# Optimization experiments

Hardware: AMD Instinct MI355X
Metric: run time of the kernel (lower is better)

The kernel has to match this reference:

```python
import jax, jax.numpy as jnp
import numpy as np

H = 64  # hidden_size

def _lstm_layer(x_tbi, h0, c0, w_ih, w_hh, b_ih, b_hh):
    """x_tbi: [T,B,I]; returns (out [T,B,H], h_n [B,H], c_n [B,H]).
    PyTorch gate order: i, f, g, o."""
    b = b_ih + b_hh  # [4H]
    # Precompute input projections for all timesteps at once (memory-friendly GEMM)
    xg = jnp.einsum('tbi,gi->tbg', x_tbi, w_ih) + b  # [T,B,4H]

    def step(carry, xg_t):
        h, c = carry
        gates = xg_t + h @ w_hh.T  # [B,4H]
        i, f, g, o = jnp.split(gates, 4, axis=-1)
        i = jax.nn.sigmoid(i)
        f = jax.nn.sigmoid(f)
        g = jnp.tanh(g)
        o = jax.nn.sigmoid(o)
        c = f * c + i * g
        h = o * jnp.tanh(c)
        return (h, c), h

    (h_n, c_n), out = jax.lax.scan(step, (h0, c0), xg)
    return out, h_n, c_n


def setup_inputs() -> dict:
    key = jax.random.key(0)
    B, T, I, O = 256, 1024, 128, 128
    ks = jax.random.split(key, 12)
    s_ih0 = 1.0 / np.sqrt(H)
    inp = {
        'x': jax.random.normal(ks[0], (B, T, I), dtype=jnp.float32),
        'h0': jnp.zeros((2, B, H), dtype=jnp.float32),
        'c0': jnp.zeros((2, B, H), dtype=jnp.float32),
        'w_ih0': jax.random.uniform(ks[1], (4 * H, I), jnp.float32, -s_ih0, s_ih0),
        'w_hh0': jax.random.uniform(ks[2], (4 * H, H), jnp.float32, -s_ih0, s_ih0),
        'b_ih0': jax.random.uniform(ks[3], (4 * H,), jnp.float32, -s_ih0, s_ih0),
        'b_hh0': jax.random.uniform(ks[4], (4 * H,), jnp.float32, -s_ih0, s_ih0),
        'w_ih1': jax.random.uniform(ks[5], (4 * H, H), jnp.float32, -s_ih0, s_ih0),
        'w_hh1': jax.random.uniform(ks[6], (4 * H, H), jnp.float32, -s_ih0, s_ih0),
        'b_ih1': jax.random.uniform(ks[7], (4 * H,), jnp.float32, -s_ih0, s_ih0),
        'b_hh1': jax.random.uniform(ks[8], (4 * H,), jnp.float32, -s_ih0, s_ih0),
        'w_fc': jax.random.uniform(ks[9], (O, H), jnp.float32, -s_ih0, s_ih0),
        'b_fc': jax.random.uniform(ks[10], (O,), jnp.float32, -s_ih0, s_ih0),
    }
    return inp


def reference(x, h0, c0, w_ih0, w_hh0, b_ih0, b_hh0, w_ih1, w_hh1, b_ih1, b_hh1, w_fc, b_fc):
    # x: [B,T,I] (batch_first) -> time-major [T,B,I]
    x_tbi = jnp.swapaxes(x, 0, 1)
    out0, h0n, c0n = _lstm_layer(x_tbi, h0[0], c0[0], w_ih0, w_hh0, b_ih0, b_hh0)
    # Dropout(p=0.5) between layers is identity in eval mode.
    out1, h1n, c1n = _lstm_layer(out0, h0[1], c0[1], w_ih1, w_hh1, b_ih1, b_hh1)
    out = jnp.swapaxes(out1, 0, 1)  # [B,T,H]
    flat = out.reshape(-1, H)  # [B*T, H]
    logits = flat @ w_fc.T + b_fc  # [B*T, O]
    h_n = jnp.stack([h0n, h1n], axis=0)  # [2,B,H]
    c_n = jnp.stack([c0n, c1n], axis=0)
    return logits, (h_n, c_n)
```

## Files before the change

kernel.cpp:

```cpp
#include <hip/hip_runtime.h>

#define T_STEPS 1024
#define BATCH   256
#define HSZ     64
#define OSZ     128

__device__ __forceinline__ float fast_rcp(float x) { return __builtin_amdgcn_rcpf(x); }
__device__ __forceinline__ float tanhf_(float x) {
    float e = __expf(2.0f * x);
    return fmaf(-2.0f, fast_rcp(e + 1.0f), 1.0f);
}


extern "C" __global__ void __launch_bounds__(512, 2)
lstm_l0(const float* __restrict__ x,
        const float* __restrict__ h0,
        const float* __restrict__ c0,
        const float* __restrict__ w_ih,
        const float* __restrict__ w_hh,
        const float* __restrict__ b_ih,
        const float* __restrict__ b_hh,
        float* __restrict__ out0,
        float* __restrict__ hn, float* __restrict__ cn)
{
    const int t_ = threadIdx.x;
    const int b  = blockIdx.x;
    const int j  = t_ >> 3;
    const int gt = (t_ >> 1) & 3;
    const int hf = t_ & 1;
    const int row = gt * HSZ + j;

    __shared__ __align__(16) float xbuf[64 * 128];
    __shared__ __align__(16) float obuf[64 * HSZ];
    __shared__ __align__(16) float hbuf[2][HSZ];

    float wih[64], whh[32];
    {
        const float4* wr = reinterpret_cast<const float4*>(w_ih + (size_t)row * 128 + hf * 64);
        #pragma unroll
        for (int k = 0; k < 16; ++k) { float4 v = wr[k];
            wih[4*k+0]=v.x; wih[4*k+1]=v.y; wih[4*k+2]=v.z; wih[4*k+3]=v.w; }
        const float4* wr2 = reinterpret_cast<const float4*>(w_hh + (size_t)row * 64 + hf * 32);
        #pragma unroll
        for (int k = 0; k < 8; ++k) { float4 v = wr2[k];
            whh[4*k+0]=v.x; whh[4*k+1]=v.y; whh[4*k+2]=v.z; whh[4*k+3]=v.w; }
    }
    const float bias = b_ih[row] + b_hh[row];
    const float am = (gt == 2) ? -2.0f : -1.0f;
    const float aa = (gt == 2) ?  2.0f :  1.0f;
    const float ab = (gt == 2) ? -1.0f :  0.0f;

    float c = c0[(size_t)b * HSZ + j];
    float h = 0.0f;
    if ((t_ & 7) == 0) hbuf[0][j] = h0[(size_t)b * HSZ + j];

    for (int t = 0; t < T_STEPS; ++t) {
        const int tc = t & 63;
        const int p  = t & 1;
        if (tc == 0) {
            if (t) {
                float4* dst = reinterpret_cast<float4*>(out0 + ((size_t)b * T_STEPS + (t - 64)) * HSZ);
                const float4* s4 = reinterpret_cast<const float4*>(obuf);
                #pragma unroll
                for (int k = 0; k < 2; ++k) dst[t_ + 512 * k] = s4[t_ + 512 * k];
            }
            const float4* src = reinterpret_cast<const float4*>(x + ((size_t)b * T_STEPS + t) * 128);
            float4* dxt = reinterpret_cast<float4*>(xbuf);
            #pragma unroll
            for (int k = 0; k < 4; ++k) dxt[t_ + 512 * k] = src[t_ + 512 * k];
            __syncthreads();
        }

        const float4* xv = reinterpret_cast<const float4*>(xbuf + tc * 128 + hf * 64);
        const float4* hv = reinterpret_cast<const float4*>(&hbuf[p][hf * 32]);
        float a0 = 0.f, a1 = 0.f, a2 = 0.f, a3 = 0.f;
        #pragma unroll
        for (int k = 0; k < 16; ++k) { float4 v = xv[k];
            a0 = fmaf(v.x, wih[4*k+0], a0);
            a1 = fmaf(v.y, wih[4*k+1], a1);
            a2 = fmaf(v.z, wih[4*k+2], a2);
            a3 = fmaf(v.w, wih[4*k+3], a3); }
        #pragma unroll
        for (int k = 0; k < 8; ++k) { float4 v = hv[k];
            a0 = fmaf(v.x, whh[4*k+0], a0);
            a1 = fmaf(v.y, whh[4*k+1], a1);
            a2 = fmaf(v.z, whh[4*k+2], a2);
            a3 = fmaf(v.w, whh[4*k+3], a3); }
        float part = (a0 + a1) + (a2 + a3);
        float pre  = part + __shfl_xor(part, 1) + bias;

        float act = fmaf(aa, fast_rcp(1.0f + __expf(am * pre)), ab);

        float q1 = __shfl_xor(act, 2);
        float q2 = __shfl_xor(act, 4);
        float q3 = __shfl_xor(q1, 4);
        const bool b0 = (gt & 1), b1 = (gt & 2);
        float lo  = b0 ? q1  : act;
        float hi  = b0 ? q3  : q2;
        float lo2 = b0 ? act : q1;
        float hi2 = b0 ? q2  : q3;
        float iv = b1 ? hi  : lo;
        float fv = b1 ? hi2 : lo2;
        float gv = b1 ? lo  : hi;
        float ov = b1 ? lo2 : hi2;

        c = fmaf(fv, c, iv * gv);
        h = ov * tanhf_(c);
        if ((t_ & 7) == 0) { hbuf[p ^ 1][j] = h; obuf[tc * HSZ + j] = h; }
        __syncthreads();
    }

    {
        float4* dst = reinterpret_cast<float4*>(out0 + ((size_t)b * T_STEPS + (T_STEPS - 64)) * HSZ);
        const float4* s4 = reinterpret_cast<const float4*>(obuf);
        #pragma unroll
        for (int k = 0; k < 2; ++k) dst[t_ + 512 * k] = s4[t_ + 512 * k];
    }
    if ((t_ & 7) == 0) {
        hn[(size_t)b * HSZ + j] = h;
        cn[(size_t)b * HSZ + j] = c;
    }
}

extern "C" __global__ void __launch_bounds__(512, 2)
lstm_l1_fc(const float* __restrict__ in0,
           const float* __restrict__ h0, const float* __restrict__ c0,
           const float* __restrict__ w_ih,
           const float* __restrict__ w_hh,
           const float* __restrict__ b_ih, const float* __restrict__ b_hh,
           const float* __restrict__ w_fc,
           const float* __restrict__ b_fc,
           float* __restrict__ logits,
           float* __restrict__ hn, float* __restrict__ cn)
{
    const int t_ = threadIdx.x;
    const int b  = blockIdx.x;
    const int j  = t_ >> 3;
    const int gt = (t_ >> 1) & 3;
    const int hf = t_ & 1;
    const int row = gt * HSZ + j;
    const int o  = t_ >> 2;
    const int q  = t_ & 3;

    __shared__ __align__(16) float ibuf[64 * HSZ];
    __shared__ __align__(16) float lbuf[64 * OSZ];
    __shared__ __align__(16) float hbuf[2][HSZ];

    float wih[32], whh[32], wfc[16];
    {
        const float4* wr = reinterpret_cast<const float4*>(w_ih + (size_t)row * 64 + hf * 32);
        #pragma unroll
        for (int k = 0; k < 8; ++k) { float4 v = wr[k];
            wih[4*k+0]=v.x; wih[4*k+1]=v.y; wih[4*k+2]=v.z; wih[4*k+3]=v.w; }
        const float4* wr2 = reinterpret_cast<const float4*>(w_hh + (size_t)row * 64 + hf * 32);
        #pragma unroll
        for (int k = 0; k < 8; ++k) { float4 v = wr2[k];
            whh[4*k+0]=v.x; whh[4*k+1]=v.y; whh[4*k+2]=v.z; whh[4*k+3]=v.w; }
        const float4* wr3 = reinterpret_cast<const float4*>(w_fc + (size_t)o * 64 + q * 16);
        #pragma unroll
        for (int k = 0; k < 4; ++k) { float4 v = wr3[k];
            wfc[4*k+0]=v.x; wfc[4*k+1]=v.y; wfc[4*k+2]=v.z; wfc[4*k+3]=v.w; }
    }
    const float bias = b_ih[row] + b_hh[row];
    const float bfc  = b_fc[o];
    const float am = (gt == 2) ? -2.0f : -1.0f;
    const float aa = (gt == 2) ?  2.0f :  1.0f;
    const float ab = (gt == 2) ? -1.0f :  0.0f;

    float c = c0[(size_t)b * HSZ + j];
    float h = 0.0f;
    if ((t_ & 7) == 0) hbuf[0][j] = h0[(size_t)b * HSZ + j];

    for (int t = 0; t < T_STEPS; ++t) {
        const int tc = t & 63;
        const int p  = t & 1;

        if (t) {
            float f0 = 0.f;
            const float4* hv4 = reinterpret_cast<const float4*>(&hbuf[p][q * 16]);
            #pragma unroll
            for (int k = 0; k < 4; ++k) { float4 v = hv4[k];
                f0 = fmaf(v.x, wfc[4*k+0], f0);
                f0 = fmaf(v.y, wfc[4*k+1], f0);
                f0 = fmaf(v.z, wfc[4*k+2], f0);
                f0 = fmaf(v.w, wfc[4*k+3], f0); }
            f0 += __shfl_xor(f0, 1);
            f0 += __shfl_xor(f0, 2);
            int slot = (tc == 0) ? 63 : (tc - 1);
            if (q == 0) lbuf[slot * OSZ + o] = f0 + bfc;
        }

        if (tc == 0) {
            if (t) {
                __syncthreads();
                float4* dst = reinterpret_cast<float4*>(logits + ((size_t)b * T_STEPS + (t - 64)) * OSZ);
                const float4* s4 = reinterpret_cast<const float4*>(lbuf);
                #pragma unroll
                for (int k = 0; k < 4; ++k) dst[t_ + 512 * k] = s4[t_ + 512 * k];
            }
            const float4* src = reinterpret_cast<const float4*>(in0 + ((size_t)b * T_STEPS + t) * HSZ);
            float4* dxt = reinterpret_cast<float4*>(ibuf);
            #pragma unroll
            for (int k = 0; k < 2; ++k) dxt[t_ + 512 * k] = src[t_ + 512 * k];
            __syncthreads();
        }

        const float4* xv = reinterpret_cast<const float4*>(ibuf + tc * HSZ + hf * 32);
        const float4* hv = reinterpret_cast<const float4*>(&hbuf[p][hf * 32]);
        float a0 = 0.f, a1 = 0.f, a2 = 0.f, a3 = 0.f;
        #pragma unroll
        for (int k = 0; k < 8; ++k) { float4 v = xv[k];
            a0 = fmaf(v.x, wih[4*k+0], a0);
            a1 = fmaf(v.y, wih[4*k+1], a1);
            a2 = fmaf(v.z, wih[4*k+2], a2);
            a3 = fmaf(v.w, wih[4*k+3], a3); }
        #pragma unroll
        for (int k = 0; k < 8; ++k) { float4 v = hv[k];
            a0 = fmaf(v.x, whh[4*k+0], a0);
            a1 = fmaf(v.y, whh[4*k+1], a1);
            a2 = fmaf(v.z, whh[4*k+2], a2);
            a3 = fmaf(v.w, whh[4*k+3], a3); }
        float part = (a0 + a1) + (a2 + a3);
        float pre  = part + __shfl_xor(part, 1) + bias;

        float act = fmaf(aa, fast_rcp(1.0f + __expf(am * pre)), ab);
        float q1 = __shfl_xor(act, 2);
        float q2 = __shfl_xor(act, 4);
        float q3 = __shfl_xor(q1, 4);
        const bool b0 = (gt & 1), b1 = (gt & 2);
        float lo  = b0 ? q1  : act;
        float hi  = b0 ? q3  : q2;
        float lo2 = b0 ? act : q1;
        float hi2 = b0 ? q2  : q3;
        float iv = b1 ? hi  : lo;
        float fv = b1 ? hi2 : lo2;
        float gv = b1 ? lo  : hi;
        float ov = b1 ? lo2 : hi2;

        c = fmaf(fv, c, iv * gv);
        h = ov * tanhf_(c);
        if ((t_ & 7) == 0) hbuf[p ^ 1][j] = h;
        __syncthreads();
    }

    {
        float f0 = 0.f;
        const float4* hv4 = reinterpret_cast<const float4*>(&hbuf[0][q * 16]);
        #pragma unroll
        for (int k = 0; k < 4; ++k) { float4 v = hv4[k];
            f0 = fmaf(v.x, wfc[4*k+0], f0);
            f0 = fmaf(v.y, wfc[4*k+1], f0);
            f0 = fmaf(v.z, wfc[4*k+2], f0);
            f0 = fmaf(v.w, wfc[4*k+3], f0); }
        f0 += __shfl_xor(f0, 1);
        f0 += __shfl_xor(f0, 2);
        if (q == 0) lbuf[63 * OSZ + o] = f0 + bfc;
        __syncthreads();
        float4* dst = reinterpret_cast<float4*>(logits + ((size_t)b * T_STEPS + (T_STEPS - 64)) * OSZ);
        const float4* s4 = reinterpret_cast<const float4*>(lbuf);
        #pragma unroll
        for (int k = 0; k < 4; ++k) dst[t_ + 512 * k] = s4[t_ + 512 * k];
    }
    if ((t_ & 7) == 0) {
        hn[(size_t)b * HSZ + j] = h;
        cn[(size_t)b * HSZ + j] = c;
    }
}

extern "C" void kernel_launch(void* const* d_in, const int* in_sizes, int n_in,
                              void* d_out, int out_size, void* d_ws, size_t ws_size,
                              hipStream_t stream) {
    const float* x     = (const float*)d_in[0];
    const float* h0    = (const float*)d_in[1];
    const float* c0    = (const float*)d_in[2];
    const float* w_ih0 = (const float*)d_in[3];
    const float* w_hh0 = (const float*)d_in[4];
    const float* b_ih0 = (const float*)d_in[5];
    const float* b_hh0 = (const float*)d_in[6];
    const float* w_ih1 = (const float*)d_in[7];
    const float* w_hh1 = (const float*)d_in[8];
    const float* b_ih1 = (const float*)d_in[9];
    const float* b_hh1 = (const float*)d_in[10];
    const float* w_fc  = (const float*)d_in[11];
    const float* b_fc  = (const float*)d_in[12];

    float* out = (float*)d_out;
    const size_t n_logits = (size_t)BATCH * T_STEPS * OSZ;
    const size_t n_state  = (size_t)BATCH * HSZ;
    float* logits = out;
    float* hn     = out + n_logits;
    float* cn     = hn + 2 * n_state;

    float* out0 = (float*)d_ws;

    lstm_l0<<<BATCH, 512, 0, stream>>>(
        x, h0, c0, w_ih0, w_hh0, b_ih0, b_hh0, out0, hn, cn);

    lstm_l1_fc<<<BATCH, 512, 0, stream>>>(
        out0, h0 + n_state, c0 + n_state,
        w_ih1, w_hh1, b_ih1, b_hh1, w_fc, b_fc,
        logits, hn + n_state, cn + n_state);
}
```

Before: 1.817 ms.

## Split block into scan and producer warps to pipeline input projection off critical path

```diff
diff --git a/kernel.cpp b/kernel.cpp
--- a/kernel.cpp
+++ b/kernel.cpp
@@ -1,122 +1,145 @@
 #include <hip/hip_runtime.h>
 
 #define T_STEPS 1024
-#define BATCH   256
 #define HSZ     64
 #define OSZ     128
 
+typedef float4 F4;
+
 __device__ __forceinline__ float fast_rcp(float x) { return __builtin_amdgcn_rcpf(x); }
-__device__ __forceinline__ float tanhf_(float x) {
+__device__ __forceinline__ float tanh_fast(float x) {
     float e = __expf(2.0f * x);
     return fmaf(-2.0f, fast_rcp(e + 1.0f), 1.0f);
 }
 
+#define DOT(W, i) { F4 v_ = vs[i]; \
+    a0 = fmaf(v_.x, (W).x, a0); a1 = fmaf(v_.y, (W).y, a1); \
+    a2 = fmaf(v_.z, (W).z, a2); a3 = fmaf(v_.w, (W).w, a3); }
+
+#define GATE_SELECT(act, gt, iv, fv, gv, ov) \
+    float q1 = __shfl_xor((act), 1); \
+    float q2 = __shfl_xor((act), 2); \
+    float q3 = __shfl_xor(q1, 2); \
+    const bool b0 = (gt) & 1, b1 = (gt) & 2; \
+    float iv = b1 ? (b0 ? q3 : q2) : (b0 ? q1 : (act)); \
+    float fv = b1 ? (b0 ? q2 : q3) : (b0 ? (act) : q1); \
+    float gv = b1 ? (b0 ? q1 : (act)) : (b0 ? q3 : q2); \
+    float ov = b1 ? (b0 ? (act) : q1) : (b0 ? q2 : q3);
 
 extern "C" __global__ void __launch_bounds__(512, 2)
 lstm_l0(const float* __restrict__ x,
-        const float* __restrict__ h0,
-        const float* __restrict__ c0,
+        const float* __restrict__ h0, const float* __restrict__ c0,
         const float* __restrict__ w_ih,
         const float* __restrict__ w_hh,
-        const float* __restrict__ b_ih,
-        const float* __restrict__ b_hh,
+        const float* __restrict__ b_ih, const float* __restrict__ b_hh,
         float* __restrict__ out0,
         float* __restrict__ hn, float* __restrict__ cn)
 {
     const int t_ = threadIdx.x;
     const int b  = blockIdx.x;
-    const int j  = t_ >> 3;
-    const int gt = (t_ >> 1) & 3;
-    const int hf = t_ & 1;
-    const int row = gt * HSZ + j;
+    const bool isScan = (t_ < 256);
+    const int u  = t_ & 255;
+    const int j  = u >> 2;
+    const int gt = u & 3;
 
     __shared__ __align__(16) float xbuf[64 * 128];
-    __shared__ __align__(16) float obuf[64 * HSZ];
+    __shared__ __align__(16) float obuf[2][64 * HSZ];
+    __shared__ __align__(16) float xg[2][256];
     __shared__ __align__(16) float hbuf[2][HSZ];
 
-    float wih[64], whh[32];
-    {
-        const float4* wr = reinterpret_cast<const float4*>(w_ih + (size_t)row * 128 + hf * 64);
-        #pragma unroll
-        for (int k = 0; k < 16; ++k) { float4 v = wr[k];
-            wih[4*k+0]=v.x; wih[4*k+1]=v.y; wih[4*k+2]=v.z; wih[4*k+3]=v.w; }
-        const float4* wr2 = reinterpret_cast<const float4*>(w_hh + (size_t)row * 64 + hf * 32);
-        #pragma unroll
-        for (int k = 0; k < 8; ++k) { float4 v = wr2[k];
-            whh[4*k+0]=v.x; whh[4*k+1]=v.y; whh[4*k+2]=v.z; whh[4*k+3]=v.w; }
-    }
-    const float bias = b_ih[row] + b_hh[row];
+    F4 W00,W01,W02,W03,W04,W05,W06,W07,W08,W09,W10,W11,W12,W13,W14,W15;
+    F4 W16,W17,W18,W19,W20,W21,W22,W23,W24,W25,W26,W27,W28,W29,W30,W31;
+    {
+        const F4 z = {0.f, 0.f, 0.f, 0.f};
+        if (isScan) {
+            const F4* ws = reinterpret_cast<const F4*>(w_hh + (size_t)(gt * HSZ + j) * HSZ);
+            W00=ws[0]; W01=ws[1]; W02=ws[2];  W03=ws[3];  W04=ws[4];  W05=ws[5];  W06=ws[6];  W07=ws[7];
+            W08=ws[8]; W09=ws[9]; W10=ws[10]; W11=ws[11]; W12=ws[12]; W13=ws[13]; W14=ws[14]; W15=ws[15];
+            W16=z; W17=z; W18=z; W19=z; W20=z; W21=z; W22=z; W23=z;
+            W24=z; W25=z; W26=z; W27=z; W28=z; W29=z; W30=z; W31=z;
+        } else {
+            const F4* ws = reinterpret_cast<const F4*>(w_ih + (size_t)u * 128);
+            W00=ws[0];  W01=ws[1];  W02=ws[2];  W03=ws[3];  W04=ws[4];  W05=ws[5];  W06=ws[6];  W07=ws[7];
+            W08=ws[8];  W09=ws[9];  W10=ws[10]; W11=ws[11]; W12=ws[12]; W13=ws[13]; W14=ws[14]; W15=ws[15];
+            W16=ws[16]; W17=ws[17]; W18=ws[18]; W19=ws[19]; W20=ws[20]; W21=ws[21]; W22=ws[22]; W23=ws[23];
+            W24=ws[24]; W25=ws[25]; W26=ws[26]; W27=ws[27]; W28=ws[28]; W29=ws[29]; W30=ws[30]; W31=ws[31];
+        }
+    }
+    const float bias = isScan ? 0.f : (b_ih[u] + b_hh[u]);
     const float am = (gt == 2) ? -2.0f : -1.0f;
     const float aa = (gt == 2) ?  2.0f :  1.0f;
     const float ab = (gt == 2) ? -1.0f :  0.0f;
 
-    float c = c0[(size_t)b * HSZ + j];
-    float h = 0.0f;
-    if ((t_ & 7) == 0) hbuf[0][j] = h0[(size_t)b * HSZ + j];
+    float c = 0.f, h = 0.f;
+    if (isScan) {
+        c = c0[(size_t)b * HSZ + j];
+        if (gt == 0) hbuf[0][j] = h0[(size_t)b * HSZ + j];
+    }
+    {
+        const F4* src = reinterpret_cast<const F4*>(x + (size_t)b * T_STEPS * 128);
+        F4* dst = reinterpret_cast<F4*>(xbuf);
+        #pragma unroll
+        for (int k = 0; k < 4; ++k) dst[t_ + 512 * k] = src[t_ + 512 * k];
+    }
+    __syncthreads();
+    if (!isScan) {
+        const F4* vs = reinterpret_cast<const F4*>(xbuf);
+        float a0=0.f,a1=0.f,a2=0.f,a3=0.f;
+        DOT(W00,0)  DOT(W01,1)  DOT(W02,2)  DOT(W03,3)  DOT(W04,4)  DOT(W05,5)  DOT(W06,6)  DOT(W07,7)
+        DOT(W08,8)  DOT(W09,9)  DOT(W10,10) DOT(W11,11) DOT(W12,12) DOT(W13,13) DOT(W14,14) DOT(W15,15)
+        DOT(W16,16) DOT(W17,17) DOT(W18,18) DOT(W19,19) DOT(W20,20) DOT(W21,21) DOT(W22,22) DOT(W23,23)
+        DOT(W24,24) DOT(W25,25) DOT(W26,26) DOT(W27,27) DOT(W28,28) DOT(W29,29) DOT(W30,30) DOT(W31,31)
+        xg[0][u] = bias + (a0 + a1) + (a2 + a3);
+    }
+    __syncthreads();
 
     for (int t = 0; t < T_STEPS; ++t) {
-        const int tc = t & 63;
-        const int p  = t & 1;
-        if (tc == 0) {
-            if (t) {
-                float4* dst = reinterpret_cast<float4*>(out0 + ((size_t)b * T_STEPS + (t - 64)) * HSZ);
-                const float4* s4 = reinterpret_cast<const float4*>(obuf);
+        if (((t & 63) == 63) && t < 1023) {
+            const F4* src = reinterpret_cast<const F4*>(x + ((size_t)b * T_STEPS + t + 1) * 128);
+            F4* dst = reinterpret_cast<F4*>(xbuf);
+            #pragma unroll
+            for (int k = 0; k < 4; ++k) dst[t_ + 512 * k] = src[t_ + 512 * k];
+            __syncthreads();
+        }
+        const int p = t & 1;
+        if (isScan) {
+            const F4* vs = reinterpret_cast<const F4*>(hbuf[p]);
+            float a0=0.f,a1=0.f,a2=0.f,a3=0.f;
+            DOT(W00,0)  DOT(W01,1)  DOT(W02,2)  DOT(W03,3)  DOT(W04,4)  DOT(W05,5)  DOT(W06,6)  DOT(W07,7)
+            DOT(W08,8)  DOT(W09,9)  DOT(W10,10) DOT(W11,11) DOT(W12,12) DOT(W13,13) DOT(W14,14) DOT(W15,15)
+            float pre = xg[p][gt * HSZ + j] + (a0 + a1) + (a2 + a3);
+            float act = fmaf(aa, fast_rcp(1.0f + __expf(am * pre)), ab);
+            GATE_SELECT(act, gt, iv, fv, gv, ov)
+            c = fmaf(fv, c, iv * gv);
+            h = ov * tanh_fast(c);
+            if (gt == 0) { hbuf[p ^ 1][j] = h; obuf[(t >> 6) & 1][(t & 63) * HSZ + j] = h; }
+        } else {
+            if (t < 1023) {
+                const F4* vs = reinterpret_cast<const F4*>(xbuf + ((t + 1) & 63) * 128);
+                float a0=0.f,a1=0.f,a2=0.f,a3=0.f;
+                DOT(W00,0)  DOT(W01,1)  DOT(W02,2)  DOT(W03,3)  DOT(W04,4)  DOT(W05,5)  DOT(W06,6)  DOT(W07,7)
+                DOT(W08,8)  DOT(W09,9)  DOT(W10,10) DOT(W11,11) DOT(W12,12) DOT(W13,13) DOT(W14,14) DOT(W15,15)
+                DOT(W16,16) DOT(W17,17) DOT(W18,18) DOT(W19,19) DOT(W20,20) DOT(W21,21) DOT(W22,22) DOT(W23,23)
+                DOT(W24,24) DOT(W25,25) DOT(W26,26) DOT(W27,27) DOT(W28,28) DOT(W29,29) DOT(W30,30) DOT(W31,31)
+                xg[p ^ 1][u] = bias + (a0 + a1) + (a2 + a3);
+            }
+            if ((t & 63) == 1 && t > 64) {
+                const int cc = (t >> 6) - 1;
+                const F4* s4 = reinterpret_cast<const F4*>(obuf[cc & 1]);
+                F4* dst = reinterpret_cast<F4*>(out0 + ((size_t)b * T_STEPS + cc * 64) * HSZ);
                 #pragma unroll
-                for (int k = 0; k < 2; ++k) dst[t_ + 512 * k] = s4[t_ + 512 * k];
-            }
-            const float4* src = reinterpret_cast<const float4*>(x + ((size_t)b * T_STEPS + t) * 128);
-            float4* dxt = reinterpret_cast<float4*>(xbuf);
-            #pragma unroll
-            for (int k = 0; k < 4; ++k) dxt[t_ + 512 * k] = src[t_ + 512 * k];
-            __syncthreads();
-        }
-
-        const float4* xv = reinterpret_cast<const float4*>(xbuf + tc * 128 + hf * 64);
-        const float4* hv = reinterpret_cast<const float4*>(&hbuf[p][hf * 32]);
-        float a0 = 0.f, a1 = 0.f, a2 = 0.f, a3 = 0.f;
-        #pragma unroll
-        for (int k = 0; k < 16; ++k) { float4 v = xv[k];
-            a0 = fmaf(v.x, wih[4*k+0], a0);
-            a1 = fmaf(v.y, wih[4*k+1], a1);
-            a2 = fmaf(v.z, wih[4*k+2], a2);
-            a3 = fmaf(v.w, wih[4*k+3], a3); }
-        #pragma unroll
-        for (int k = 0; k < 8; ++k) { float4 v = hv[k];
-            a0 = fmaf(v.x, whh[4*k+0], a0);
-            a1 = fmaf(v.y, whh[4*k+1], a1);
-            a2 = fmaf(v.z, whh[4*k+2], a2);
-            a3 = fmaf(v.w, whh[4*k+3], a3); }
-        float part = (a0 + a1) + (a2 + a3);
-        float pre  = part + __shfl_xor(part, 1) + bias;
-
-        float act = fmaf(aa, fast_rcp(1.0f + __expf(am * pre)), ab);
-
-        float q1 = __shfl_xor(act, 2);
-        float q2 = __shfl_xor(act, 4);
-        float q3 = __shfl_xor(q1, 4);
-        const bool b0 = (gt & 1), b1 = (gt & 2);
-        float lo  = b0 ? q1  : act;
-        float hi  = b0 ? q3  : q2;
-        float lo2 = b0 ? act : q1;
-        float hi2 = b0 ? q2  : q3;
-        float iv = b1 ? hi  : lo;
-        float fv = b1 ? hi2 : lo2;
-        float gv = b1 ? lo  : hi;
-        float ov = b1 ? lo2 : hi2;
-
-        c = fmaf(fv, c, iv * gv);
-        h = ov * tanhf_(c);
-        if ((t_ & 7) == 0) { hbuf[p ^ 1][j] = h; obuf[tc * HSZ + j] = h; }
+                for (int k = 0; k < 4; ++k) dst[u + 256 * k] = s4[u + 256 * k];
+            }
+        }
         __syncthreads();
     }
-
-    {
-        float4* dst = reinterpret_cast<float4*>(out0 + ((size_t)b * T_STEPS + (T_STEPS - 64)) * HSZ);
-        const float4* s4 = reinterpret_cast<const float4*>(obuf);
+    {
+        const F4* s4 = reinterpret_cast<const F4*>(obuf[1]);
+        F4* dst = reinterpret_cast<F4*>(out0 + ((size_t)b * T_STEPS + 15 * 64) * HSZ);
         #pragma unroll
         for (int k = 0; k < 2; ++k) dst[t_ + 512 * k] = s4[t_ + 512 * k];
     }
-    if ((t_ & 7) == 0) {
+    if (isScan && gt == 0) {
         hn[(size_t)b * HSZ + j] = h;
         cn[(size_t)b * HSZ + j] = c;
     }
@@ -135,133 +158,124 @@
 {
     const int t_ = threadIdx.x;
     const int b  = blockIdx.x;
-    const int j  = t_ >> 3;
-    const int gt = (t_ >> 1) & 3;
-    const int hf = t_ & 1;
-    const int row = gt * HSZ + j;
-    const int o  = t_ >> 2;
-    const int q  = t_ & 3;
+    const bool isScan = (t_ < 256);
+    const int u  = t_ & 255;
+    const int j  = u >> 2;
+    const int gt = u & 3;
+    const int o  = u >> 1;
+    const int hh = u & 1;
 
     __shared__ __align__(16) float ibuf[64 * HSZ];
-    __shared__ __align__(16) float lbuf[64 * OSZ];
+    __shared__ __align__(16) float lbuf[2][64 * OSZ];
+    __shared__ __align__(16) float xg[2][256];
     __shared__ __align__(16) float hbuf[2][HSZ];
 
-    float wih[32], whh[32], wfc[16];
-    {
-        const float4* wr = reinterpret_cast<const float4*>(w_ih + (size_t)row * 64 + hf * 32);
-        #pragma unroll
-        for (int k = 0; k < 8; ++k) { float4 v = wr[k];
-            wih[4*k+0]=v.x; wih[4*k+1]=v.y; wih[4*k+2]=v.z; wih[4*k+3]=v.w; }
-        const float4* wr2 = reinterpret_cast<const float4*>(w_hh + (size_t)row * 64 + hf * 32);
-        #pragma unroll
-        for (int k = 0; k < 8; ++k) { float4 v = wr2[k];
-            whh[4*k+0]=v.x; whh[4*k+1]=v.y; whh[4*k+2]=v.z; whh[4*k+3]=v.w; }
-        const float4* wr3 = reinterpret_cast<const float4*>(w_fc + (size_t)o * 64 + q * 16);
-        #pragma unroll
-        for (int k = 0; k < 4; ++k) { float4 v = wr3[k];
-            wfc[4*k+0]=v.x; wfc[4*k+1]=v.y; wfc[4*k+2]=v.z; wfc[4*k+3]=v.w; }
-    }
-    const float bias = b_ih[row] + b_hh[row];
+    F4 W00,W01,W02,W03,W04,W05,W06,W07,W08,W09,W10,W11,W12,W13,W14,W15;
+    F4 W16,W17,W18,W19,W20,W21,W22,W23;
+    {
+        if (isScan) {
+            const F4 z = {0.f, 0.f, 0.f, 0.f};
+            const F4* ws = reinterpret_cast<const F4*>(w_hh + (size_t)(gt * HSZ + j) * HSZ);
+            W00=ws[0]; W01=ws[1]; W02=ws[2];  W03=ws[3];  W04=ws[4];  W05=ws[5];  W06=ws[6];  W07=ws[7];
+            W08=ws[8]; W09=ws[9]; W10=ws[10]; W11=ws[11]; W12=ws[12]; W13=ws[13]; W14=ws[14]; W15=ws[15];
+            W16=z; W17=z; W18=z; W19=z; W20=z; W21=z; W22=z; W23=z;
+        } else {
+            const F4* ws = reinterpret_cast<const F4*>(w_ih + (size_t)u * HSZ);
+            W00=ws[0]; W01=ws[1]; W02=ws[2];  W03=ws[3];  W04=ws[4];  W05=ws[5];  W06=ws[6];  W07=ws[7];
+            W08=ws[8]; W09=ws[9]; W10=ws[10]; W11=ws[11]; W12=ws[12]; W13=ws[13]; W14=ws[14]; W15=ws[15];
+            const F4* wf = reinterpret_cast<const F4*>(w_fc + (size_t)o * HSZ + hh * 32);
+            W16=wf[0]; W17=wf[1]; W18=wf[2]; W19=wf[3]; W20=wf[4]; W21=wf[5]; W22=wf[6]; W23=wf[7];
+        }
+    }
+    const float bias = isScan ? 0.f : (b_ih[u] + b_hh[u]);
     const float bfc  = b_fc[o];
     const float am = (gt == 2) ? -2.0f : -1.0f;
     const float aa = (gt == 2) ?  2.0f :  1.0f;
     const float ab = (gt == 2) ? -1.0f :  0.0f;
 
-    float c = c0[(size_t)b * HSZ + j];
-    float h = 0.0f;
-    if ((t_ & 7) == 0) hbuf[0][j] = h0[(size_t)b * HSZ + j];
+    float c = 0.f, h = 0.f;
+    if (isScan) {
+        c = c0[(size_t)b * HSZ + j];
+        if (gt == 0) hbuf[0][j] = h0[(size_t)b * HSZ + j];
+    }
+    {
+        const F4* src = reinterpret_cast<const F4*>(in0 + (size_t)b * T_STEPS * HSZ);
+        F4* dst = reinterpret_cast<F4*>(ibuf);
+        #pragma unroll
+        for (int k = 0; k < 2; ++k) dst[t_ + 512 * k] = src[t_ + 512 * k];
+    }
+    __syncthreads();
+    if (!isScan) {
+        const F4* vs = reinterpret_cast<const F4*>(ibuf);
+        float a0=0.f,a1=0.f,a2=0.f,a3=0.f;
+        DOT(W00,0)  DOT(W01,1)  DOT(W02,2)  DOT(W03,3)  DOT(W04,4)  DOT(W05,5)  DOT(W06,6)  DOT(W07,7)
+        DOT(W08,8)  DOT(W09,9)  DOT(W10,10) DOT(W11,11) DOT(W12,12) DOT(W13,13) DOT(W14,14) DOT(W15,15)
+        xg[0][u] = bias + (a0 + a1) + (a2 + a3);
+    }
+    __syncthreads();
 
     for (int t = 0; t < T_STEPS; ++t) {
-        const int tc = t & 63;
-        const int p  = t & 1;
-
-        if (t) {
-            float f0 = 0.f;
-            const float4* hv4 = reinterpret_cast<const float4*>(&hbuf[p][q * 16]);
+        if (((t & 63) == 63) && t < 1023) {
+            const F4* src = reinterpret_cast<const F4*>(in0 + ((size_t)b * T_STEPS + t + 1) * HSZ);
+            F4* dst = reinterpret_cast<F4*>(ibuf);
             #pragma unroll
-            for (int k = 0; k < 4; ++k) { float4 v = hv4[k];
-                f0 = fmaf(v.x, wfc[4*k+0], f0);
-                f0 = fmaf(v.y, wfc[4*k+1], f0);
-                f0 = fmaf(v.z, wfc[4*k+2], f0);
-                f0 = fmaf(v.w, wfc[4*k+3], f0); }
-            f0 += __shfl_xor(f0, 1);
-            f0 += __shfl_xor(f0, 2);
-            int slot = (tc == 0) ? 63 : (tc - 1);
-            if (q == 0) lbuf[slot * OSZ + o] = f0 + bfc;
-        }
-
-        if (tc == 0) {
-            if (t) {
-                __syncthreads();
-                float4* dst = reinterpret_cast<float4*>(logits + ((size_t)b * T_STEPS + (t - 64)) * OSZ);
-                const float4* s4 = reinterpret_cast<const float4*>(lbuf);
+            for (int k = 0; k < 2; ++k) dst[t_ + 512 * k] = src[t_ + 512 * k];
+            __syncthreads();
+        }
+        const int p = t & 1;
+        if (isScan) {
+            const F4* vs = reinterpret_cast<const F4*>(hbuf[p]);
+            float a0=0.f,a1=0.f,a2=0.f,a3=0.f;
+            DOT(W00,0)  DOT(W01,1)  DOT(W02,2)  DOT(W03,3)  DOT(W04,4)  DOT(W05,5)  DOT(W06,6)  DOT(W07,7)
+            DOT(W08,8)  DOT(W09,9)  DOT(W10,10) DOT(W11,11) DOT(W12,12) DOT(W13,13) DOT(W14,14) DOT(W15,15)
+            float pre = xg[p][gt * HSZ + j] + (a0 + a1) + (a2 + a3);
+            float act = fmaf(aa, fast_rcp(1.0f + __expf(am * pre)), ab);
+            GATE_SELECT(act, gt, iv, fv, gv, ov)
+            c = fmaf(fv, c, iv * gv);
+            h = ov * tanh_fast(c);
+            if (gt == 0) hbuf[p ^ 1][j] = h;
+        } else {
+            if (t < 1023) {
+                const F4* vs = reinterpret_cast<const F4*>(ibuf + ((t + 1) & 63) * HSZ);
+                float a0=0.f,a1=0.f,a2=0.f,a3=0.f;
+                DOT(W00,0)  DOT(W01,1)  DOT(W02,2)  DOT(W03,3)  DOT(W04,4)  DOT(W05,5)  DOT(W06,6)  DOT(W07,7)
+                DOT(W08,8)  DOT(W09,9)  DOT(W10,10) DOT(W11,11) DOT(W12,12) DOT(W13,13) DOT(W14,14) DOT(W15,15)
+                xg[p ^ 1][u] = bias + (a0 + a1) + (a2 + a3);
+            }
+            if (t > 0) {
+                const F4* vs = reinterpret_cast<const F4*>(&hbuf[p][hh * 32]);
+                float a0=0.f,a1=0.f,a2=0.f,a3=0.f;
+                DOT(W16,0) DOT(W17,1) DOT(W18,2) DOT(W19,3) DOT(W20,4) DOT(W21,5) DOT(W22,6) DOT(W23,7)
+                float f = (a0 + a1) + (a2 + a3);
+                f += __shfl_xor(f, 1);
+                if (hh == 0) lbuf[((t - 1) >> 6) & 1][((t - 1) & 63) * OSZ + o] = f + bfc;
+            }
+            if ((t & 63) == 1 && t > 64) {
+                const int cc = (t >> 6) - 1;
+                const F4* s4 = reinterpret_cast<const F4*>(lbuf[cc & 1]);
+                F4* dst = reinterpret_cast<F4*>(logits + ((size_t)b * T_STEPS + cc * 64) * OSZ);
                 #pragma unroll
-                for (int k = 0; k < 4; ++k) dst[t_ + 512 * k] = s4[t_ + 512 * k];
-            }
-            const float4* src = reinterpret_cast<const float4*>(in0 + ((size_t)b * T_STEPS + t) * HSZ);
-            float4* dxt = reinterpret_cast<float4*>(ibuf);
-            #pragma unroll
-            for (int k = 0; k < 2; ++k) dxt[t_ + 512 * k] = src[t_ + 512 * k];
-            __syncthreads();
-        }
-
-        const float4* xv = reinterpret_cast<const float4*>(ibuf + tc * HSZ + hf * 32);
-        const float4* hv = reinterpret_cast<const float4*>(&hbuf[p][hf * 32]);
-        float a0 = 0.f, a1 = 0.f, a2 = 0.f, a3 = 0.f;
-        #pragma unroll
-        for (int k = 0; k < 8; ++k) { float4 v = xv[k];
-            a0 = fmaf(v.x, wih[4*k+0], a0);
-            a1 = fmaf(v.y, wih[4*k+1], a1);
-            a2 = fmaf(v.z, wih[4*k+2], a2);
-            a3 = fmaf(v.w, wih[4*k+3], a3); }
-        #pragma unroll
-        for (int k = 0; k < 8; ++k) { float4 v = hv[k];
-            a0 = fmaf(v.x, whh[4*k+0], a0);
-            a1 = fmaf(v.y, whh[4*k+1], a1);
-            a2 = fmaf(v.z, whh[4*k+2], a2);
-            a3 = fmaf(v.w, whh[4*k+3], a3); }
-        float part = (a0 + a1) + (a2 + a3);
-        float pre  = part + __shfl_xor(part, 1) + bias;
-
-        float act = fmaf(aa, fast_rcp(1.0f + __expf(am * pre)), ab);
-        float q1 = __shfl_xor(act, 2);
-        float q2 = __shfl_xor(act, 4);
-        float q3 = __shfl_xor(q1, 4);
-        const bool b0 = (gt & 1), b1 = (gt & 2);
-        float lo  = b0 ? q1  : act;
-        float hi  = b0 ? q3  : q2;
-        float lo2 = b0 ? act : q1;
-        float hi2 = b0 ? q2  : q3;
-        float iv = b1 ? hi  : lo;
-        float fv = b1 ? hi2 : lo2;
-        float gv = b1 ? lo  : hi;
-        float ov = b1 ? lo2 : hi2;
-
-        c = fmaf(fv, c, iv * gv);
-        h = ov * tanhf_(c);
-        if ((t_ & 7) == 0) hbuf[p ^ 1][j] = h;
+                for (int k = 0; k < 8; ++k) dst[u + 256 * k] = s4[u + 256 * k];
+            }
+        }
         __syncthreads();
     }
-
-    {
-        float f0 = 0.f;
-        const float4* hv4 = reinterpret_cast<const float4*>(&hbuf[0][q * 16]);
-        #pragma unroll
-        for (int k = 0; k < 4; ++k) { float4 v = hv4[k];
-            f0 = fmaf(v.x, wfc[4*k+0], f0);
-            f0 = fmaf(v.y, wfc[4*k+1], f0);
-            f0 = fmaf(v.z, wfc[4*k+2], f0);
-            f0 = fmaf(v.w, wfc[4*k+3], f0); }
-        f0 += __shfl_xor(f0, 1);
-        f0 += __shfl_xor(f0, 2);
-        if (q == 0) lbuf[63 * OSZ + o] = f0 + bfc;
-        __syncthreads();
-        float4* dst = reinterpret_cast<float4*>(logits + ((size_t)b * T_STEPS + (T_STEPS - 64)) * OSZ);
-        const float4* s4 = reinterpret_cast<const float4*>(lbuf);
+    if (!isScan) {
+        const F4* vs = reinterpret_cast<const F4*>(&hbuf[0][hh * 32]);
+        float a0=0.f,a1=0.f,a2=0.f,a3=0.f;
+        DOT(W16,0) DOT(W17,1) DOT(W18,2) DOT(W19,3) DOT(W20,4) DOT(W21,5) DOT(W22,6) DOT(W23,7)
+        float f = (a0 + a1) + (a2 + a3);
+        f += __shfl_xor(f, 1);
+        if (hh == 0) lbuf[1][63 * OSZ + o] = f + bfc;
+    }
+    __syncthreads();
+    {
+        const F4* s4 = reinterpret_cast<const F4*>(lbuf[1]);
+        F4* dst = reinterpret_cast<F4*>(logits + ((size_t)b * T_STEPS + 15 * 64) * OSZ);
         #pragma unroll
         for (int k = 0; k < 4; ++k) dst[t_ + 512 * k] = s4[t_ + 512 * k];
     }
-    if ((t_ & 7) == 0) {
+    if (isScan && gt == 0) {
         hn[(size_t)b * HSZ + j] = h;
         cn[(size_t)b * HSZ + j] = c;
     }
@@ -285,18 +299,18 @@
     const float* b_fc  = (const float*)d_in[12];
 
     float* out = (float*)d_out;
-    const size_t n_logits = (size_t)BATCH * T_STEPS * OSZ;
-    const size_t n_state  = (size_t)BATCH * HSZ;
+    const size_t n_logits = (size_t)256 * T_STEPS * OSZ;
+    const size_t n_state  = (size_t)256 * HSZ;
     float* logits = out;
     float* hn     = out + n_logits;
     float* cn     = hn + 2 * n_state;
 
     float* out0 = (float*)d_ws;
 
-    lstm_l0<<<BATCH, 512, 0, stream>>>(
+    lstm_l0<<<256, 512, 0, stream>>>(
         x, h0, c0, w_ih0, w_hh0, b_ih0, b_hh0, out0, hn, cn);
 
-    lstm_l1_fc<<<BATCH, 512, 0, stream>>>(
+    lstm_l1_fc<<<256, 512, 0, stream>>>(
         out0, h0 + n_state, c0 + n_state,
         w_ih1, w_hh1, b_ih1, b_hh1, w_fc, b_fc,
         logits, hn + n_state, cn + n_state);
```

Result: slower. 1.863 ms (+2.5%).
